# Kernel tuning notes

Hardware: AMD Instinct MI355X
Metric: run time of the kernel (lower is better)

Reference implementation:

```python
import jax, jax.numpy as jnp
import numpy as np

SEQ = 4096
NUM_INP = 1024
NUM_OUT = 128
NUM_HEADS = 8
NUM_HIDDEN = 64  # hardcoded in __init__
LN_EPS = 1e-5


def setup_inputs() -> dict:
    key = jax.random.key(0)
    ks = jax.random.split(key, 7)
    d_kq = NUM_HEADS * NUM_HIDDEN
    d_v = NUM_HEADS * NUM_OUT
    lim = 1.0 / np.sqrt(NUM_INP)
    return {
        "x": jax.random.normal(ks[0], (SEQ, NUM_INP), dtype=jnp.float32),
        "Wk": jax.random.uniform(ks[1], (d_kq, NUM_INP), jnp.float32, -lim, lim),
        "bk": jax.random.uniform(ks[2], (d_kq,), jnp.float32, -lim, lim),
        "Wq": jax.random.uniform(ks[3], (d_kq, NUM_INP), jnp.float32, -lim, lim),
        "bq": jax.random.uniform(ks[4], (d_kq,), jnp.float32, -lim, lim),
        "Wv": jax.random.uniform(ks[5], (d_v, NUM_INP), jnp.float32, -lim, lim),
        "bv": jax.random.uniform(ks[6], (d_v,), jnp.float32, -lim, lim),
        "ln_w": jnp.ones((NUM_OUT,), jnp.float32),
        "ln_b": jnp.zeros((NUM_OUT,), jnp.float32),
    }


def reference(x, Wk, bk, Wq, bq, Wv, bv, ln_w, ln_b):
    S = x.shape[0]
    # projections (eqx.nn.Linear: y = W @ x + b)
    k = (x @ Wk.T + bk).reshape(S, NUM_HEADS, NUM_HIDDEN)
    k = k / jnp.sqrt(jnp.asarray(NUM_HIDDEN, k.dtype))
    q = (x @ Wq.T + bq).reshape(S, NUM_HEADS, NUM_HIDDEN)
    v = (x @ Wv.T + bv).reshape(S, NUM_HEADS, NUM_OUT)
    # logits[i, j, h] = sum_k keys[i,h,k] * queries[j,h,k]
    logits = jnp.einsum('ihk,jhk->ijh', k, q)
    # softmax over axis=1 (the j / query axis, as in the original)
    attn = jax.nn.softmax(logits, axis=1)
    # contract over j AND heads -> [S, NUM_OUT]
    out = jnp.einsum('ijh,jhe->ie', attn, v)
    # LayerNorm over last dim with affine params
    mu = jnp.mean(out, axis=-1, keepdims=True)
    var = jnp.var(out, axis=-1, keepdims=True)
    normed = (out - mu) / jnp.sqrt(var + LN_EPS)
    return normed * ln_w + ln_b
```

## Files before the change

kernel.cpp:

```cpp
#include <hip/hip_runtime.h>
#include <hip/hip_bf16.h>

#define SEQ   4096
#define NINP  1024
#define NH    8
#define ND    64
#define NE    128
#define DKQ   512
#define DV    1024

typedef __attribute__((ext_vector_type(8))) short  short8;
typedef __attribute__((ext_vector_type(4))) float  floatx4;
typedef __attribute__((ext_vector_type(4))) unsigned short ushortx4;

__device__ __forceinline__ unsigned short f2bf(float f) {
    union { float f; unsigned int i; } v; v.f = f;
    unsigned int r = v.i + 0x7fffu + ((v.i >> 16) & 1u);
    return (unsigned short)(r >> 16);
}
__device__ __forceinline__ unsigned int pkperm(float hi, float lo) {
    return __builtin_amdgcn_perm(__float_as_uint(hi), __float_as_uint(lo), 0x07060302u);
}
__device__ __forceinline__ short8 pk8p(float4 a, float4 b) {
    int4 w;
    w.x = (int)pkperm(a.y, a.x);
    w.y = (int)pkperm(a.w, a.z);
    w.z = (int)pkperm(b.y, b.x);
    w.w = (int)pkperm(b.w, b.z);
    return *(short8*)&w;
}
__device__ __forceinline__ floatx4 mfma16(short8 a, short8 b, floatx4 c) {
    return __builtin_amdgcn_mfma_f32_16x16x32_bf16(a, b, c, 0, 0, 0);
}

__global__ __launch_bounds__(256)
void conv_kernel(const float* __restrict__ x,  const float* __restrict__ Wk,
                 const float* __restrict__ Wq, const float* __restrict__ Wv,
                 unsigned short* __restrict__ xbf,  unsigned short* __restrict__ Wkbf,
                 unsigned short* __restrict__ Wqbf, unsigned short* __restrict__ Wvbf)
{
    size_t idx = (size_t)blockIdx.x * 256 + threadIdx.x;
    const float* src; unsigned short* dst; size_t off;
    if      (idx < 524288)  { src = x;  dst = xbf;  off = idx; }
    else if (idx < 589824)  { src = Wk; dst = Wkbf; off = idx - 524288; }
    else if (idx < 655360)  { src = Wq; dst = Wqbf; off = idx - 589824; }
    else                    { src = Wv; dst = Wvbf; off = idx - 655360; }
    float4 a = *(const float4*)(src + off * 8);
    float4 b = *(const float4*)(src + off * 8 + 4);
    *(short8*)(dst + off * 8) = pk8p(a, b);
}

__global__ __launch_bounds__(256, 2)
void proj_kernel(const unsigned short* __restrict__ xbf,
                 const unsigned short* __restrict__ Wkbf, const float* __restrict__ bk,
                 const unsigned short* __restrict__ Wqbf, const float* __restrict__ bq,
                 const unsigned short* __restrict__ Wvbf, const float* __restrict__ bvv,
                 unsigned short* __restrict__ Kbuf, unsigned short* __restrict__ Qfrag,
                 unsigned short* __restrict__ Vfrag)
{
    __shared__ unsigned short As[128][72];
    __shared__ unsigned short Bs[128][72];

    const int ct = blockIdx.x;
    const int m0 = blockIdx.y * 128;

    const unsigned short* W; const float* bias;
    int colbase; float scale; int dest;
    if (ct < 4)      { W = Wkbf; bias = bk;  colbase = ct * 128;       scale = 0.18033688f; dest = 0; }
    else if (ct < 8) { W = Wqbf; bias = bq;  colbase = (ct - 4) * 128; scale = 1.0f;        dest = 1; }
    else             { W = Wvbf; bias = bvv; colbase = (ct - 8) * 128; scale = 1.0f;        dest = 2; }

    const int tid  = threadIdx.x;
    const int wv   = tid >> 6;
    const int lane = tid & 63;
    const int n    = lane & 15;
    const int qd   = lane >> 4;
    const int wr   = wv >> 1, wc = wv & 1;
    const int sr   = tid >> 1;
    const int skc  = (tid & 1) * 32;

    const unsigned short* xa0 = xbf + (size_t)(m0 + sr) * NINP + skc;
    const unsigned short* wb0 = W + (size_t)(colbase + sr) * NINP + skc;

    floatx4 acc[4][4] = {};
    short8 px[4], pw[4];

    #pragma unroll
    for (int c = 0; c < 4; ++c) {
        px[c] = *(const short8*)(xa0 + c*8);
        pw[c] = *(const short8*)(wb0 + c*8);
    }

    for (int k0 = 0; k0 < NINP; k0 += 64) {
        #pragma unroll
        for (int c = 0; c < 4; ++c) {
            *(short8*)&As[sr][skc + c*8] = px[c];
            *(short8*)&Bs[sr][skc + c*8] = pw[c];
        }
        const int kn = (k0 + 64 < NINP) ? k0 + 64 : k0;
        #pragma unroll
        for (int c = 0; c < 4; ++c) {
            px[c] = *(const short8*)(xa0 + kn + c*8);
            pw[c] = *(const short8*)(wb0 + kn + c*8);
        }
        __syncthreads();
        #pragma unroll
        for (int kk = 0; kk < 2; ++kk) {
            short8 af[4], bf4[4];
            #pragma unroll
            for (int mi = 0; mi < 4; ++mi)
                af[mi] = *(const short8*)&As[wr*64 + mi*16 + n][kk*32 + qd*8];
            #pragma unroll
            for (int ni = 0; ni < 4; ++ni)
                bf4[ni] = *(const short8*)&Bs[wc*64 + ni*16 + n][kk*32 + qd*8];
            #pragma unroll
            for (int mi = 0; mi < 4; ++mi)
                #pragma unroll
                for (int ni = 0; ni < 4; ++ni)
                    acc[mi][ni] = mfma16(af[mi], bf4[ni], acc[mi][ni]);
        }
        __syncthreads();
    }

    #pragma unroll
    for (int mi = 0; mi < 4; ++mi) {
        #pragma unroll
        for (int ni = 0; ni < 4; ++ni) {
            int o = colbase + wc*64 + ni*16 + n;
            float bfv = bias[o];
            int srow = m0 + wr*64 + mi*16 + qd*4;
            if (dest == 2) {
                int hh = o >> 7, e = o & 127;
                int e16 = e >> 4, ne = e & 15;
                int jt = srow >> 5, qd_a = (srow >> 3) & 3, t0 = srow & 7;
                ushortx4 pkv;
                #pragma unroll
                for (int r = 0; r < 4; ++r) pkv[r] = f2bf(acc[mi][ni][r] + bfv);
                *(ushortx4*)(Vfrag + (((size_t)hh*128 + jt)*8 + e16)*512
                             + (qd_a*16 + ne)*8 + t0) = pkv;
            } else if (dest == 1) {
                int hh = o >> 6, d = o & 63;
                int dd = d >> 5, qd_l = (d >> 3) & 3, t = d & 7;
                int jt = srow >> 5, a = (srow >> 4) & 1;
                size_t base = (((size_t)hh*128 + jt)*4 + (a + 2*dd))*512 + t;
                #pragma unroll
                for (int r = 0; r < 4; ++r) {
                    int nl = (srow + r) & 15;
                    Qfrag[base + (qd_l*16 + nl)*8] = f2bf(acc[mi][ni][r] + bfv);
                }
            } else {
                #pragma unroll
                for (int r = 0; r < 4; ++r)
                    Kbuf[(size_t)(srow + r) * DKQ + o] = f2bf((acc[mi][ni][r] + bfv) * scale);
            }
        }
    }
}

__global__ __launch_bounds__(256, 4)
void attn_kernel(const unsigned short* __restrict__ Kbuf,
                 const unsigned short* __restrict__ Qfrag,
                 const unsigned short* __restrict__ Vfrag,
                 float* __restrict__ Obuf,
                 float* dout)
{
    __shared__ unsigned char smem[34816];
    float* Red  = (float*)smem;
    float* DenS = (float*)(smem + 2 * 32 * 132 * 4);

    const int b    = blockIdx.x;
    const int h    = b & 7;
    const int i0   = (b >> 3) * 32;
    const int tid  = threadIdx.x;
    const int j_q  = tid >> 6;
    const int lane = tid & 63;
    const int n    = lane & 15;
    const int qd   = lane >> 4;

    short8 kf[2][2];
    #pragma unroll
    for (int g = 0; g < 2; ++g)
        #pragma unroll
        for (int d = 0; d < 2; ++d)
            kf[g][d] = *(const short8*)(Kbuf + (size_t)(i0 + g*16 + n) * DKQ
                                        + h * ND + d*32 + qd*8);

    floatx4 acc[8][2] = {};
    float den[2] = {0.f, 0.f};

    const int adA = (((qd & 1) << 5) + n) * 4;
    const int adB = adA + 64;
    const bool lo = (qd < 2);

    const unsigned short* Qbase = Qfrag + (size_t)h * 128 * 4 * 512 + lane * 8;
    const unsigned short* Vbase = Vfrag + (size_t)h * 128 * 8 * 512 + lane * 8;

    for (int k = 0; k < 32; ++k) {
        const int jt = j_q * 32 + k;

        const unsigned short* Qb = Qbase + (size_t)jt * 4 * 512;
        short8 qf00 = *(const short8*)(Qb);
        short8 qf10 = *(const short8*)(Qb + 512);
        short8 qf01 = *(const short8*)(Qb + 1024);
        short8 qf11 = *(const short8*)(Qb + 1536);
        const unsigned short* Vb = Vbase + (size_t)jt * 8 * 512;
        short8 vf[8];
        #pragma unroll
        for (int e16 = 0; e16 < 8; ++e16)
            vf[e16] = *(const short8*)(Vb + e16 * 512);

        floatx4 s[2][2] = {};
        #pragma unroll
        for (int g = 0; g < 2; ++g) {
            s[0][g] = mfma16(qf00, kf[g][0], s[0][g]); s[0][g] = mfma16(qf01, kf[g][1], s[0][g]);
            s[1][g] = mfma16(qf10, kf[g][0], s[1][g]); s[1][g] = mfma16(qf11, kf[g][1], s[1][g]);
        }

        int pkk[2][2][2];
        #pragma unroll
        for (int a = 0; a < 2; ++a)
            #pragma unroll
            for (int g = 0; g < 2; ++g) {
                float p0 = __builtin_amdgcn_exp2f(s[a][g][0]);
                float p1 = __builtin_amdgcn_exp2f(s[a][g][1]);
                float p2 = __builtin_amdgcn_exp2f(s[a][g][2]);
                float p3 = __builtin_amdgcn_exp2f(s[a][g][3]);
                den[g] += (p0 + p1) + (p2 + p3);
                pkk[a][g][0] = (int)pkperm(p1, p0);
                pkk[a][g][1] = (int)pkperm(p3, p2);
            }

        short8 bfrag[2];
        #pragma unroll
        for (int g = 0; g < 2; ++g) {
            int w0a = __builtin_amdgcn_ds_bpermute(adA, pkk[0][g][0]);
            int w1a = __builtin_amdgcn_ds_bpermute(adA, pkk[0][g][1]);
            int w2a = __builtin_amdgcn_ds_bpermute(adB, pkk[0][g][0]);
            int w3a = __builtin_amdgcn_ds_bpermute(adB, pkk[0][g][1]);
            int w0b = __builtin_amdgcn_ds_bpermute(adA, pkk[1][g][0]);
            int w1b = __builtin_amdgcn_ds_bpermute(adA, pkk[1][g][1]);
            int w2b = __builtin_amdgcn_ds_bpermute(adB, pkk[1][g][0]);
            int w3b = __builtin_amdgcn_ds_bpermute(adB, pkk[1][g][1]);
            int4 wv4;
            wv4.x = lo ? w0a : w0b;
            wv4.y = lo ? w1a : w1b;
            wv4.z = lo ? w2a : w2b;
            wv4.w = lo ? w3a : w3b;
            bfrag[g] = *(short8*)&wv4;
        }

        #pragma unroll
        for (int e16 = 0; e16 < 8; ++e16) {
            acc[e16][0] = mfma16(vf[e16], bfrag[0], acc[e16][0]);
            acc[e16][1] = mfma16(vf[e16], bfrag[1], acc[e16][1]);
        }
    }

    #pragma unroll
    for (int g = 0; g < 2; ++g) {
        den[g] += __shfl_xor(den[g], 16);
        den[g] += __shfl_xor(den[g], 32);
    }
    if (lane < 16) {
        DenS[j_q*32 + 0  + lane] = den[0];
        DenS[j_q*32 + 16 + lane] = den[1];
    }

    if (j_q >= 2) {
        #pragma unroll
        for (int e16 = 0; e16 < 8; ++e16)
            #pragma unroll
            for (int g = 0; g < 2; ++g)
                *(floatx4*)&Red[(j_q - 2)*32*132 + (g*16 + n)*132 + e16*16 + qd*4] = acc[e16][g];
    }
    __syncthreads();
    if (j_q == 1) {
        #pragma unroll
        for (int e16 = 0; e16 < 8; ++e16)
            #pragma unroll
            for (int g = 0; g < 2; ++g) {
                float* p = &Red[1*32*132 + (g*16 + n)*132 + e16*16 + qd*4];
                floatx4 o = *(const floatx4*)p;
                acc[e16][g][0] += o[0]; acc[e16][g][1] += o[1];
                acc[e16][g][2] += o[2]; acc[e16][g][3] += o[3];
                *(floatx4*)p = acc[e16][g];
            }
    } else if (j_q == 0) {
        #pragma unroll
        for (int e16 = 0; e16 < 8; ++e16)
            #pragma unroll
            for (int g = 0; g < 2; ++g) {
                floatx4 o = *(const floatx4*)&Red[0*32*132 + (g*16 + n)*132 + e16*16 + qd*4];
                acc[e16][g][0] += o[0]; acc[e16][g][1] += o[1];
                acc[e16][g][2] += o[2]; acc[e16][g][3] += o[3];
            }
    }
    __syncthreads();
    if (j_q == 0) {
        #pragma unroll
        for (int e16 = 0; e16 < 8; ++e16)
            #pragma unroll
            for (int g = 0; g < 2; ++g) {
                floatx4 o = *(const floatx4*)&Red[1*32*132 + (g*16 + n)*132 + e16*16 + qd*4];
                acc[e16][g][0] += o[0]; acc[e16][g][1] += o[1];
                acc[e16][g][2] += o[2]; acc[e16][g][3] += o[3];
                float* dst = Obuf + ((size_t)h * SEQ + i0 + g*16 + n) * NE + e16*16 + qd*4;
                *(floatx4*)dst = acc[e16][g];
            }
        if (lane < 32)
            dout[(size_t)(i0 + lane) * NE + h] =
                DenS[lane] + DenS[32 + lane] + DenS[64 + lane] + DenS[96 + lane];
    }
}

__global__ __launch_bounds__(256)
void ln_kernel(const float* __restrict__ Obuf,
               const float* __restrict__ lnA,
               const float* __restrict__ lnB,
               float* out)
{
    const bool aIsW = (lnA[0] == 1.0f);
    const float* lw = aIsW ? lnA : lnB;
    const float* lb = aIsW ? lnB : lnA;

    const int i    = blockIdx.x * 4 + (threadIdx.x >> 6);
    const int lane = threadIdx.x & 63;
    const int e0   = lane * 2;

    float inv[8];
    #pragma unroll
    for (int h = 0; h < 8; ++h) inv[h] = 1.0f / out[(size_t)i * NE + h];

    float x0 = 0.f, x1 = 0.f;
    #pragma unroll
    for (int h = 0; h < 8; ++h) {
        const float* p = Obuf + ((size_t)h * SEQ + i) * NE + e0;
        x0 += p[0] * inv[h]; x1 += p[1] * inv[h];
    }
    float s = x0 + x1, s2 = x0*x0 + x1*x1;
    #pragma unroll
    for (int off = 1; off < 64; off <<= 1) {
        s  += __shfl_xor(s,  off);
        s2 += __shfl_xor(s2, off);
    }
    float mu   = s * (1.f / 128.f);
    float var  = s2 * (1.f / 128.f) - mu * mu;
    float rstd = rsqrtf(var + 1e-5f);
    float2 y;
    y.x = (x0 - mu) * rstd * lw[e0]     + lb[e0];
    y.y = (x1 - mu) * rstd * lw[e0 + 1] + lb[e0 + 1];
    *(float2*)(out + (size_t)i * NE + e0) = y;
}

extern "C" void kernel_launch(void* const* d_in, const int* in_sizes, int n_in,
                              void* d_out, int out_size, void* d_ws, size_t ws_size,
                              hipStream_t stream)
{
    long long smax = 0;
    for (int i = 0; i < n_in; ++i) if ((long long)in_sizes[i] > smax) smax = in_sizes[i];
    const float *x = nullptr, *Wk = nullptr, *Wq = nullptr, *Wv = nullptr;
    const float *bk = nullptr, *bq = nullptr, *bv = nullptr, *lnA = nullptr, *lnB = nullptr;
    for (int i = 0; i < n_in; ++i) {
        long long s = in_sizes[i];
        const float* p = (const float*)d_in[i];
        if      (s == smax)          { x = p; }
        else if (s * 4 == smax)      { Wv = p; }
        else if (s * 8 == smax)      { if (!Wk) Wk = p; else Wq = p; }
        else if (s * 4096 == smax)   { bv = p; }
        else if (s * 8192 == smax)   { if (!bk) bk = p; else bq = p; }
        else if (s * 32768 == smax)  { if (!lnA) lnA = p; else lnB = p; }
    }

    unsigned short* Kbuf  = (unsigned short*)d_ws;
    unsigned short* Qfrag = Kbuf + (size_t)SEQ * DKQ;
    unsigned short* Vfrag = Qfrag + (size_t)SEQ * DKQ;
    unsigned short* xbf   = Vfrag + (size_t)NH * NE * SEQ;
    unsigned short* Wkbf  = xbf + (size_t)SEQ * NINP;
    unsigned short* Wqbf  = Wkbf + (size_t)DKQ * NINP;
    unsigned short* Wvbf  = Wqbf + (size_t)DKQ * NINP;
    float*          Obuf  = (float*)xbf;
    float*          out   = (float*)d_out;

    conv_kernel<<<dim3(3072), 256, 0, stream>>>(x, Wk, Wq, Wv, xbf, Wkbf, Wqbf, Wvbf);
    proj_kernel<<<dim3(16, 32), 256, 0, stream>>>(xbf, Wkbf, bk, Wqbf, bq, Wvbf, bv,
                                                  Kbuf, Qfrag, Vfrag);
    attn_kernel<<<dim3(1024), 256, 0, stream>>>(Kbuf, Qfrag, Vfrag, Obuf, out);
    ln_kernel<<<dim3(1024), 256, 0, stream>>>(Obuf, lnA, lnB, out);
}
```

Before: 203.3 us.

## Double attention row tile per block to reuse Q/V fragments across 64 rows

Each attention block now covers 64 key rows instead of 32, halving the grid to 512 blocks. The Q and V fragments loaded per j-tile are therefore reused across four row groups, halving global/L2 traffic for Q and V. The cross-wave reduction is split into two column halves so the shared-memory footprint stays about the same. The price is more accumulator registers, a lower occupancy target (launch bounds 2), and fewer blocks to spread across the CUs.

New measurement: 171.3 us. 1.19x faster.

```diff
diff --git a/kernel.cpp b/kernel.cpp
--- a/kernel.cpp
+++ b/kernel.cpp
@@ -157,36 +157,37 @@
     }
 }
 
-__global__ __launch_bounds__(256, 4)
+__global__ __launch_bounds__(256, 2)
 void attn_kernel(const unsigned short* __restrict__ Kbuf,
                  const unsigned short* __restrict__ Qfrag,
                  const unsigned short* __restrict__ Vfrag,
                  float* __restrict__ Obuf,
                  float* dout)
 {
-    __shared__ unsigned char smem[34816];
-    float* Red  = (float*)smem;
-    float* DenS = (float*)(smem + 2 * 32 * 132 * 4);
+    __shared__ unsigned char smem[35840];
+    float* Red0 = (float*)smem;
+    float* Red1 = Red0 + 64 * 68;
+    float* DenS = Red1 + 64 * 68;
 
     const int b    = blockIdx.x;
     const int h    = b & 7;
-    const int i0   = (b >> 3) * 32;
+    const int i0   = (b >> 3) * 64;
     const int tid  = threadIdx.x;
     const int j_q  = tid >> 6;
     const int lane = tid & 63;
     const int n    = lane & 15;
     const int qd   = lane >> 4;
 
-    short8 kf[2][2];
-    #pragma unroll
-    for (int g = 0; g < 2; ++g)
+    short8 kf[4][2];
+    #pragma unroll
+    for (int g = 0; g < 4; ++g)
         #pragma unroll
         for (int d = 0; d < 2; ++d)
             kf[g][d] = *(const short8*)(Kbuf + (size_t)(i0 + g*16 + n) * DKQ
                                         + h * ND + d*32 + qd*8);
 
-    floatx4 acc[8][2] = {};
-    float den[2] = {0.f, 0.f};
+    floatx4 acc[8][4] = {};
+    float den[4] = {0.f, 0.f, 0.f, 0.f};
 
     const int adA = (((qd & 1) << 5) + n) * 4;
     const int adB = adA + 64;
@@ -198,118 +199,131 @@
     for (int k = 0; k < 32; ++k) {
         const int jt = j_q * 32 + k;
 
-        const unsigned short* Qb = Qbase + (size_t)jt * 4 * 512;
+        const unsigned short* Qb = Qbase + (size_t)jt * 2048;
         short8 qf00 = *(const short8*)(Qb);
         short8 qf10 = *(const short8*)(Qb + 512);
         short8 qf01 = *(const short8*)(Qb + 1024);
         short8 qf11 = *(const short8*)(Qb + 1536);
-        const unsigned short* Vb = Vbase + (size_t)jt * 8 * 512;
+        const unsigned short* Vb = Vbase + (size_t)jt * 4096;
         short8 vf[8];
         #pragma unroll
         for (int e16 = 0; e16 < 8; ++e16)
             vf[e16] = *(const short8*)(Vb + e16 * 512);
 
-        floatx4 s[2][2] = {};
-        #pragma unroll
-        for (int g = 0; g < 2; ++g) {
-            s[0][g] = mfma16(qf00, kf[g][0], s[0][g]); s[0][g] = mfma16(qf01, kf[g][1], s[0][g]);
-            s[1][g] = mfma16(qf10, kf[g][0], s[1][g]); s[1][g] = mfma16(qf11, kf[g][1], s[1][g]);
-        }
-
-        int pkk[2][2][2];
-        #pragma unroll
-        for (int a = 0; a < 2; ++a)
-            #pragma unroll
-            for (int g = 0; g < 2; ++g) {
-                float p0 = __builtin_amdgcn_exp2f(s[a][g][0]);
-                float p1 = __builtin_amdgcn_exp2f(s[a][g][1]);
-                float p2 = __builtin_amdgcn_exp2f(s[a][g][2]);
-                float p3 = __builtin_amdgcn_exp2f(s[a][g][3]);
-                den[g] += (p0 + p1) + (p2 + p3);
-                pkk[a][g][0] = (int)pkperm(p1, p0);
-                pkk[a][g][1] = (int)pkperm(p3, p2);
+        #pragma unroll
+        for (int gc = 0; gc < 2; ++gc) {
+            floatx4 s[2][2] = {};
+            #pragma unroll
+            for (int gi = 0; gi < 2; ++gi) {
+                const int g = gc*2 + gi;
+                s[0][gi] = mfma16(qf00, kf[g][0], s[0][gi]); s[0][gi] = mfma16(qf01, kf[g][1], s[0][gi]);
+                s[1][gi] = mfma16(qf10, kf[g][0], s[1][gi]); s[1][gi] = mfma16(qf11, kf[g][1], s[1][gi]);
             }
 
-        short8 bfrag[2];
-        #pragma unroll
-        for (int g = 0; g < 2; ++g) {
-            int w0a = __builtin_amdgcn_ds_bpermute(adA, pkk[0][g][0]);
-            int w1a = __builtin_amdgcn_ds_bpermute(adA, pkk[0][g][1]);
-            int w2a = __builtin_amdgcn_ds_bpermute(adB, pkk[0][g][0]);
-            int w3a = __builtin_amdgcn_ds_bpermute(adB, pkk[0][g][1]);
-            int w0b = __builtin_amdgcn_ds_bpermute(adA, pkk[1][g][0]);
-            int w1b = __builtin_amdgcn_ds_bpermute(adA, pkk[1][g][1]);
-            int w2b = __builtin_amdgcn_ds_bpermute(adB, pkk[1][g][0]);
-            int w3b = __builtin_amdgcn_ds_bpermute(adB, pkk[1][g][1]);
-            int4 wv4;
-            wv4.x = lo ? w0a : w0b;
-            wv4.y = lo ? w1a : w1b;
-            wv4.z = lo ? w2a : w2b;
-            wv4.w = lo ? w3a : w3b;
-            bfrag[g] = *(short8*)&wv4;
-        }
-
-        #pragma unroll
-        for (int e16 = 0; e16 < 8; ++e16) {
-            acc[e16][0] = mfma16(vf[e16], bfrag[0], acc[e16][0]);
-            acc[e16][1] = mfma16(vf[e16], bfrag[1], acc[e16][1]);
-        }
-    }
-
-    #pragma unroll
-    for (int g = 0; g < 2; ++g) {
+            int pkk[2][2][2];
+            #pragma unroll
+            for (int a = 0; a < 2; ++a)
+                #pragma unroll
+                for (int gi = 0; gi < 2; ++gi) {
+                    float p0 = __builtin_amdgcn_exp2f(s[a][gi][0]);
+                    float p1 = __builtin_amdgcn_exp2f(s[a][gi][1]);
+                    float p2 = __builtin_amdgcn_exp2f(s[a][gi][2]);
+                    float p3 = __builtin_amdgcn_exp2f(s[a][gi][3]);
+                    den[gc*2 + gi] += (p0 + p1) + (p2 + p3);
+                    pkk[a][gi][0] = (int)pkperm(p1, p0);
+                    pkk[a][gi][1] = (int)pkperm(p3, p2);
+                }
+
+            short8 bfrag[2];
+            #pragma unroll
+            for (int gi = 0; gi < 2; ++gi) {
+                int w0a = __builtin_amdgcn_ds_bpermute(adA, pkk[0][gi][0]);
+                int w1a = __builtin_amdgcn_ds_bpermute(adA, pkk[0][gi][1]);
+                int w2a = __builtin_amdgcn_ds_bpermute(adB, pkk[0][gi][0]);
+                int w3a = __builtin_amdgcn_ds_bpermute(adB, pkk[0][gi][1]);
+                int w0b = __builtin_amdgcn_ds_bpermute(adA, pkk[1][gi][0]);
+                int w1b = __builtin_amdgcn_ds_bpermute(adA, pkk[1][gi][1]);
+                int w2b = __builtin_amdgcn_ds_bpermute(adB, pkk[1][gi][0]);
+                int w3b = __builtin_amdgcn_ds_bpermute(adB, pkk[1][gi][1]);
+                int4 wv4;
+                wv4.x = lo ? w0a : w0b;
+                wv4.y = lo ? w1a : w1b;
+                wv4.z = lo ? w2a : w2b;
+                wv4.w = lo ? w3a : w3b;
+                bfrag[gi] = *(short8*)&wv4;
+            }
+
+            #pragma unroll
+            for (int e16 = 0; e16 < 8; ++e16) {
+                acc[e16][gc*2]     = mfma16(vf[e16], bfrag[0], acc[e16][gc*2]);
+                acc[e16][gc*2 + 1] = mfma16(vf[e16], bfrag[1], acc[e16][gc*2 + 1]);
+            }
+        }
+    }
+
+    #pragma unroll
+    for (int g = 0; g < 4; ++g) {
         den[g] += __shfl_xor(den[g], 16);
         den[g] += __shfl_xor(den[g], 32);
     }
     if (lane < 16) {
-        DenS[j_q*32 + 0  + lane] = den[0];
-        DenS[j_q*32 + 16 + lane] = den[1];
-    }
-
-    if (j_q >= 2) {
-        #pragma unroll
-        for (int e16 = 0; e16 < 8; ++e16)
-            #pragma unroll
-            for (int g = 0; g < 2; ++g)
-                *(floatx4*)&Red[(j_q - 2)*32*132 + (g*16 + n)*132 + e16*16 + qd*4] = acc[e16][g];
-    }
-    __syncthreads();
-    if (j_q == 1) {
-        #pragma unroll
-        for (int e16 = 0; e16 < 8; ++e16)
-            #pragma unroll
-            for (int g = 0; g < 2; ++g) {
-                float* p = &Red[1*32*132 + (g*16 + n)*132 + e16*16 + qd*4];
-                floatx4 o = *(const floatx4*)p;
-                acc[e16][g][0] += o[0]; acc[e16][g][1] += o[1];
-                acc[e16][g][2] += o[2]; acc[e16][g][3] += o[3];
-                *(floatx4*)p = acc[e16][g];
-            }
-    } else if (j_q == 0) {
-        #pragma unroll
-        for (int e16 = 0; e16 < 8; ++e16)
-            #pragma unroll
-            for (int g = 0; g < 2; ++g) {
-                floatx4 o = *(const floatx4*)&Red[0*32*132 + (g*16 + n)*132 + e16*16 + qd*4];
-                acc[e16][g][0] += o[0]; acc[e16][g][1] += o[1];
-                acc[e16][g][2] += o[2]; acc[e16][g][3] += o[3];
-            }
-    }
-    __syncthreads();
+        #pragma unroll
+        for (int g = 0; g < 4; ++g)
+            DenS[j_q*64 + g*16 + lane] = den[g];
+    }
+
+    #pragma unroll
+    for (int eh = 0; eh < 2; ++eh) {
+        if (eh) __syncthreads();
+        if (j_q >= 2) {
+            float* Rb = (j_q == 2) ? Red0 : Red1;
+            #pragma unroll
+            for (int e = 0; e < 4; ++e)
+                #pragma unroll
+                for (int g = 0; g < 4; ++g)
+                    *(floatx4*)&Rb[(g*16 + n)*68 + e*16 + qd*4] = acc[eh*4 + e][g];
+        }
+        __syncthreads();
+        if (j_q == 1) {
+            #pragma unroll
+            for (int e = 0; e < 4; ++e)
+                #pragma unroll
+                for (int g = 0; g < 4; ++g) {
+                    float* p = &Red1[(g*16 + n)*68 + e*16 + qd*4];
+                    floatx4 o = *(const floatx4*)p;
+                    floatx4 r = acc[eh*4 + e][g];
+                    r[0] += o[0]; r[1] += o[1]; r[2] += o[2]; r[3] += o[3];
+                    *(floatx4*)p = r;
+                }
+        } else if (j_q == 0) {
+            #pragma unroll
+            for (int e = 0; e < 4; ++e)
+                #pragma unroll
+                for (int g = 0; g < 4; ++g) {
+                    floatx4 o = *(const floatx4*)&Red0[(g*16 + n)*68 + e*16 + qd*4];
+                    acc[eh*4 + e][g][0] += o[0]; acc[eh*4 + e][g][1] += o[1];
+                    acc[eh*4 + e][g][2] += o[2]; acc[eh*4 + e][g][3] += o[3];
+                }
+        }
+        __syncthreads();
+        if (j_q == 0) {
+            #pragma unroll
+            for (int e = 0; e < 4; ++e)
+                #pragma unroll
+                for (int g = 0; g < 4; ++g) {
+                    floatx4 o = *(const floatx4*)&Red1[(g*16 + n)*68 + e*16 + qd*4];
+                    floatx4 r = acc[eh*4 + e][g];
+                    r[0] += o[0]; r[1] += o[1]; r[2] += o[2]; r[3] += o[3];
+                    float* dst = Obuf + ((size_t)h * SEQ + i0 + g*16 + n) * NE
+                                 + (eh*4 + e)*16 + qd*4;
+                    *(floatx4*)dst = r;
+                }
+        }
+    }
+
     if (j_q == 0) {
-        #pragma unroll
-        for (int e16 = 0; e16 < 8; ++e16)
-            #pragma unroll
-            for (int g = 0; g < 2; ++g) {
-                floatx4 o = *(const floatx4*)&Red[1*32*132 + (g*16 + n)*132 + e16*16 + qd*4];
-                acc[e16][g][0] += o[0]; acc[e16][g][1] += o[1];
-                acc[e16][g][2] += o[2]; acc[e16][g][3] += o[3];
-                float* dst = Obuf + ((size_t)h * SEQ + i0 + g*16 + n) * NE + e16*16 + qd*4;
-                *(floatx4*)dst = acc[e16][g];
-            }
-        if (lane < 32)
-            dout[(size_t)(i0 + lane) * NE + h] =
-                DenS[lane] + DenS[32 + lane] + DenS[64 + lane] + DenS[96 + lane];
+        dout[(size_t)(i0 + lane) * NE + h] =
+            DenS[lane] + DenS[64 + lane] + DenS[128 + lane] + DenS[192 + lane];
     }
 }
 
@@ -384,6 +398,6 @@
     conv_kernel<<<dim3(3072), 256, 0, stream>>>(x, Wk, Wq, Wv, xbf, Wkbf, Wqbf, Wvbf);
     proj_kernel<<<dim3(16, 32), 256, 0, stream>>>(xbf, Wkbf, bk, Wqbf, bq, Wvbf, bv,
                                                   Kbuf, Qfrag, Vfrag);
-    attn_kernel<<<dim3(1024), 256, 0, stream>>>(Kbuf, Qfrag, Vfrag, Obuf, out);
+    attn_kernel<<<dim3(512), 256, 0, stream>>>(Kbuf, Qfrag, Vfrag, Obuf, out);
     ln_kernel<<<dim3(1024), 256, 0, stream>>>(Obuf, lnA, lnB, out);
 }
```

## Give each attention wave its own query rows over all keys, drop LDS reduction

Applied to the files above, without the earlier changes.

Before, the four waves of a block split the j (key) range and combined their partial outputs through shared memory with two barriers. Now each wave owns a distinct 16-row slice of a 64-row block and walks all 128 key tiles, so the LDS reduction and syncs disappear and the grid is halved. Q and V fragment loads are double-buffered in registers to overlap the next tile's loads with the current tile's MFMAs. The costs are that each wave reads the full Q/V stream for its head, occupancy is lowered to 2 blocks per unit, and the K fragment is no longer shared between two row groups per wave.

Measured after the change: 256.6 us. 1.26x slower.

```diff
diff --git a/kernel.cpp b/kernel.cpp
--- a/kernel.cpp
+++ b/kernel.cpp
@@ -157,160 +157,103 @@
     }
 }
 
-__global__ __launch_bounds__(256, 4)
+__global__ __launch_bounds__(256, 2)
 void attn_kernel(const unsigned short* __restrict__ Kbuf,
                  const unsigned short* __restrict__ Qfrag,
                  const unsigned short* __restrict__ Vfrag,
                  float* __restrict__ Obuf,
                  float* dout)
 {
-    __shared__ unsigned char smem[34816];
-    float* Red  = (float*)smem;
-    float* DenS = (float*)(smem + 2 * 32 * 132 * 4);
-
     const int b    = blockIdx.x;
     const int h    = b & 7;
-    const int i0   = (b >> 3) * 32;
+    const int i0   = (b >> 3) * 64;
     const int tid  = threadIdx.x;
-    const int j_q  = tid >> 6;
+    const int g    = tid >> 6;
     const int lane = tid & 63;
     const int n    = lane & 15;
     const int qd   = lane >> 4;
 
-    short8 kf[2][2];
-    #pragma unroll
-    for (int g = 0; g < 2; ++g)
-        #pragma unroll
-        for (int d = 0; d < 2; ++d)
-            kf[g][d] = *(const short8*)(Kbuf + (size_t)(i0 + g*16 + n) * DKQ
-                                        + h * ND + d*32 + qd*8);
-
-    floatx4 acc[8][2] = {};
-    float den[2] = {0.f, 0.f};
+    short8 kf[2];
+    #pragma unroll
+    for (int d = 0; d < 2; ++d)
+        kf[d] = *(const short8*)(Kbuf + (size_t)(i0 + g*16 + n) * DKQ
+                                 + h * ND + d*32 + qd*8);
+
+    floatx4 acc[8] = {};
+    float den = 0.f;
 
     const int adA = (((qd & 1) << 5) + n) * 4;
     const int adB = adA + 64;
     const bool lo = (qd < 2);
 
-    const unsigned short* Qbase = Qfrag + (size_t)h * 128 * 4 * 512 + lane * 8;
-    const unsigned short* Vbase = Vfrag + (size_t)h * 128 * 8 * 512 + lane * 8;
-
-    for (int k = 0; k < 32; ++k) {
-        const int jt = j_q * 32 + k;
-
-        const unsigned short* Qb = Qbase + (size_t)jt * 4 * 512;
-        short8 qf00 = *(const short8*)(Qb);
-        short8 qf10 = *(const short8*)(Qb + 512);
-        short8 qf01 = *(const short8*)(Qb + 1024);
-        short8 qf11 = *(const short8*)(Qb + 1536);
-        const unsigned short* Vb = Vbase + (size_t)jt * 8 * 512;
-        short8 vf[8];
+    const unsigned short* Qbase = Qfrag + (size_t)h * (128*4*512) + lane * 8;
+    const unsigned short* Vbase = Vfrag + (size_t)h * (128*8*512) + lane * 8;
+
+    short8 qA[4], vA[8], qB[4], vB[8];
+
+    auto fetch = [&](short8 (&qf)[4], short8 (&vf)[8], int jt) {
+        const unsigned short* Qb = Qbase + (size_t)jt * 2048;
+        const unsigned short* Vb = Vbase + (size_t)jt * 4096;
+        #pragma unroll
+        for (int f = 0; f < 4; ++f) qf[f] = *(const short8*)(Qb + f * 512);
+        #pragma unroll
+        for (int e = 0; e < 8; ++e) vf[e] = *(const short8*)(Vb + e * 512);
+    };
+
+    auto compute = [&](const short8 (&qf)[4], const short8 (&vf)[8]) {
+        floatx4 s[2] = {};
+        s[0] = mfma16(qf[0], kf[0], s[0]); s[0] = mfma16(qf[2], kf[1], s[0]);
+        s[1] = mfma16(qf[1], kf[0], s[1]); s[1] = mfma16(qf[3], kf[1], s[1]);
+
+        int pkk[2][2];
+        #pragma unroll
+        for (int a = 0; a < 2; ++a) {
+            float p0 = __builtin_amdgcn_exp2f(s[a][0]);
+            float p1 = __builtin_amdgcn_exp2f(s[a][1]);
+            float p2 = __builtin_amdgcn_exp2f(s[a][2]);
+            float p3 = __builtin_amdgcn_exp2f(s[a][3]);
+            den += (p0 + p1) + (p2 + p3);
+            pkk[a][0] = (int)pkperm(p1, p0);
+            pkk[a][1] = (int)pkperm(p3, p2);
+        }
+
+        int w0a = __builtin_amdgcn_ds_bpermute(adA, pkk[0][0]);
+        int w1a = __builtin_amdgcn_ds_bpermute(adA, pkk[0][1]);
+        int w2a = __builtin_amdgcn_ds_bpermute(adB, pkk[0][0]);
+        int w3a = __builtin_amdgcn_ds_bpermute(adB, pkk[0][1]);
+        int w0b = __builtin_amdgcn_ds_bpermute(adA, pkk[1][0]);
+        int w1b = __builtin_amdgcn_ds_bpermute(adA, pkk[1][1]);
+        int w2b = __builtin_amdgcn_ds_bpermute(adB, pkk[1][0]);
+        int w3b = __builtin_amdgcn_ds_bpermute(adB, pkk[1][1]);
+        int4 wv4;
+        wv4.x = lo ? w0a : w0b;
+        wv4.y = lo ? w1a : w1b;
+        wv4.z = lo ? w2a : w2b;
+        wv4.w = lo ? w3a : w3b;
+        short8 bfrag = *(short8*)&wv4;
+
         #pragma unroll
         for (int e16 = 0; e16 < 8; ++e16)
-            vf[e16] = *(const short8*)(Vb + e16 * 512);
-
-        floatx4 s[2][2] = {};
-        #pragma unroll
-        for (int g = 0; g < 2; ++g) {
-            s[0][g] = mfma16(qf00, kf[g][0], s[0][g]); s[0][g] = mfma16(qf01, kf[g][1], s[0][g]);
-            s[1][g] = mfma16(qf10, kf[g][0], s[1][g]); s[1][g] = mfma16(qf11, kf[g][1], s[1][g]);
-        }
-
-        int pkk[2][2][2];
-        #pragma unroll
-        for (int a = 0; a < 2; ++a)
-            #pragma unroll
-            for (int g = 0; g < 2; ++g) {
-                float p0 = __builtin_amdgcn_exp2f(s[a][g][0]);
-                float p1 = __builtin_amdgcn_exp2f(s[a][g][1]);
-                float p2 = __builtin_amdgcn_exp2f(s[a][g][2]);
-                float p3 = __builtin_amdgcn_exp2f(s[a][g][3]);
-                den[g] += (p0 + p1) + (p2 + p3);
-                pkk[a][g][0] = (int)pkperm(p1, p0);
-                pkk[a][g][1] = (int)pkperm(p3, p2);
-            }
-
-        short8 bfrag[2];
-        #pragma unroll
-        for (int g = 0; g < 2; ++g) {
-            int w0a = __builtin_amdgcn_ds_bpermute(adA, pkk[0][g][0]);
-            int w1a = __builtin_amdgcn_ds_bpermute(adA, pkk[0][g][1]);
-            int w2a = __builtin_amdgcn_ds_bpermute(adB, pkk[0][g][0]);
-            int w3a = __builtin_amdgcn_ds_bpermute(adB, pkk[0][g][1]);
-            int w0b = __builtin_amdgcn_ds_bpermute(adA, pkk[1][g][0]);
-            int w1b = __builtin_amdgcn_ds_bpermute(adA, pkk[1][g][1]);
-            int w2b = __builtin_amdgcn_ds_bpermute(adB, pkk[1][g][0]);
-            int w3b = __builtin_amdgcn_ds_bpermute(adB, pkk[1][g][1]);
-            int4 wv4;
-            wv4.x = lo ? w0a : w0b;
-            wv4.y = lo ? w1a : w1b;
-            wv4.z = lo ? w2a : w2b;
-            wv4.w = lo ? w3a : w3b;
-            bfrag[g] = *(short8*)&wv4;
-        }
-
-        #pragma unroll
-        for (int e16 = 0; e16 < 8; ++e16) {
-            acc[e16][0] = mfma16(vf[e16], bfrag[0], acc[e16][0]);
-            acc[e16][1] = mfma16(vf[e16], bfrag[1], acc[e16][1]);
-        }
-    }
-
-    #pragma unroll
-    for (int g = 0; g < 2; ++g) {
-        den[g] += __shfl_xor(den[g], 16);
-        den[g] += __shfl_xor(den[g], 32);
-    }
-    if (lane < 16) {
-        DenS[j_q*32 + 0  + lane] = den[0];
-        DenS[j_q*32 + 16 + lane] = den[1];
-    }
-
-    if (j_q >= 2) {
-        #pragma unroll
-        for (int e16 = 0; e16 < 8; ++e16)
-            #pragma unroll
-            for (int g = 0; g < 2; ++g)
-                *(floatx4*)&Red[(j_q - 2)*32*132 + (g*16 + n)*132 + e16*16 + qd*4] = acc[e16][g];
-    }
-    __syncthreads();
-    if (j_q == 1) {
-        #pragma unroll
-        for (int e16 = 0; e16 < 8; ++e16)
-            #pragma unroll
-            for (int g = 0; g < 2; ++g) {
-                float* p = &Red[1*32*132 + (g*16 + n)*132 + e16*16 + qd*4];
-                floatx4 o = *(const floatx4*)p;
-                acc[e16][g][0] += o[0]; acc[e16][g][1] += o[1];
-                acc[e16][g][2] += o[2]; acc[e16][g][3] += o[3];
-                *(floatx4*)p = acc[e16][g];
-            }
-    } else if (j_q == 0) {
-        #pragma unroll
-        for (int e16 = 0; e16 < 8; ++e16)
-            #pragma unroll
-            for (int g = 0; g < 2; ++g) {
-                floatx4 o = *(const floatx4*)&Red[0*32*132 + (g*16 + n)*132 + e16*16 + qd*4];
-                acc[e16][g][0] += o[0]; acc[e16][g][1] += o[1];
-                acc[e16][g][2] += o[2]; acc[e16][g][3] += o[3];
-            }
-    }
-    __syncthreads();
-    if (j_q == 0) {
-        #pragma unroll
-        for (int e16 = 0; e16 < 8; ++e16)
-            #pragma unroll
-            for (int g = 0; g < 2; ++g) {
-                floatx4 o = *(const floatx4*)&Red[1*32*132 + (g*16 + n)*132 + e16*16 + qd*4];
-                acc[e16][g][0] += o[0]; acc[e16][g][1] += o[1];
-                acc[e16][g][2] += o[2]; acc[e16][g][3] += o[3];
-                float* dst = Obuf + ((size_t)h * SEQ + i0 + g*16 + n) * NE + e16*16 + qd*4;
-                *(floatx4*)dst = acc[e16][g];
-            }
-        if (lane < 32)
-            dout[(size_t)(i0 + lane) * NE + h] =
-                DenS[lane] + DenS[32 + lane] + DenS[64 + lane] + DenS[96 + lane];
-    }
+            acc[e16] = mfma16(vf[e16], bfrag, acc[e16]);
+    };
+
+    fetch(qA, vA, 0);
+    for (int jt = 0; jt < 128; jt += 2) {
+        fetch(qB, vB, jt + 1);
+        compute(qA, vA);
+        fetch(qA, vA, (jt + 2 < 128) ? jt + 2 : jt);
+        compute(qB, vB);
+    }
+
+    den += __shfl_xor(den, 16);
+    den += __shfl_xor(den, 32);
+    if (lane < 16)
+        dout[(size_t)(i0 + g*16 + lane) * NE + h] = den;
+
+    #pragma unroll
+    for (int e16 = 0; e16 < 8; ++e16)
+        *(floatx4*)(Obuf + ((size_t)h * SEQ + i0 + g*16 + n) * NE + e16*16 + qd*4)
+            = acc[e16];
 }
 
 __global__ __launch_bounds__(256)
@@ -384,6 +327,6 @@
     conv_kernel<<<dim3(3072), 256, 0, stream>>>(x, Wk, Wq, Wv, xbf, Wkbf, Wqbf, Wvbf);
     proj_kernel<<<dim3(16, 32), 256, 0, stream>>>(xbf, Wkbf, bk, Wqbf, bq, Wvbf, bv,
                                                   Kbuf, Qfrag, Vfrag);
-    attn_kernel<<<dim3(1024), 256, 0, stream>>>(Kbuf, Qfrag, Vfrag, Obuf, out);
+    attn_kernel<<<dim3(512), 256, 0, stream>>>(Kbuf, Qfrag, Vfrag, Obuf, out);
     ln_kernel<<<dim3(1024), 256, 0, stream>>>(Obuf, lnA, lnB, out);
 }
```

## Double attention block to 64 rows and split LDS reduction into halves

Applied to the files above, without the earlier changes.

The attention kernel now launches 512-thread blocks that each cover two 32-row query groups (8 waves: 2 row groups x 4 key-range waves). Waves in the same block that read the same Q/V fragments can share them through cache, and there are half as many blocks. The cross-wave reduction now runs in two halves over the output columns with a 68-float stride, so two row groups fit in about the same LDS as one did before. The cost is an extra barrier round per block, and a larger block may reduce scheduling flexibility and occupancy.

Result: no change. 201.2 us (-1.0%).

```diff
diff --git a/kernel.cpp b/kernel.cpp
--- a/kernel.cpp
+++ b/kernel.cpp
@@ -157,22 +157,24 @@
     }
 }
 
-__global__ __launch_bounds__(256, 4)
+__global__ __launch_bounds__(512, 4)
 void attn_kernel(const unsigned short* __restrict__ Kbuf,
                  const unsigned short* __restrict__ Qfrag,
                  const unsigned short* __restrict__ Vfrag,
                  float* __restrict__ Obuf,
                  float* dout)
 {
-    __shared__ unsigned char smem[34816];
+    __shared__ unsigned char smem[35840];
     float* Red  = (float*)smem;
-    float* DenS = (float*)(smem + 2 * 32 * 132 * 4);
+    float* DenS = (float*)(smem + 4 * 32 * 68 * 4);
 
     const int b    = blockIdx.x;
     const int h    = b & 7;
-    const int i0   = (b >> 3) * 32;
     const int tid  = threadIdx.x;
-    const int j_q  = tid >> 6;
+    const int w    = tid >> 6;
+    const int iq   = w >> 2;
+    const int jq   = w & 3;
+    const int i0   = (b >> 3) * 64 + iq * 32;
     const int lane = tid & 63;
     const int n    = lane & 15;
     const int qd   = lane >> 4;
@@ -196,14 +198,14 @@
     const unsigned short* Vbase = Vfrag + (size_t)h * 128 * 8 * 512 + lane * 8;
 
     for (int k = 0; k < 32; ++k) {
-        const int jt = j_q * 32 + k;
-
-        const unsigned short* Qb = Qbase + (size_t)jt * 4 * 512;
+        const int jt = jq * 32 + k;
+
+        const unsigned short* Qb = Qbase + (size_t)jt * 2048;
         short8 qf00 = *(const short8*)(Qb);
         short8 qf10 = *(const short8*)(Qb + 512);
         short8 qf01 = *(const short8*)(Qb + 1024);
         short8 qf11 = *(const short8*)(Qb + 1536);
-        const unsigned short* Vb = Vbase + (size_t)jt * 8 * 512;
+        const unsigned short* Vb = Vbase + (size_t)jt * 4096;
         short8 vf[8];
         #pragma unroll
         for (int e16 = 0; e16 < 8; ++e16)
@@ -262,54 +264,65 @@
         den[g] += __shfl_xor(den[g], 32);
     }
     if (lane < 16) {
-        DenS[j_q*32 + 0  + lane] = den[0];
-        DenS[j_q*32 + 16 + lane] = den[1];
-    }
-
-    if (j_q >= 2) {
-        #pragma unroll
-        for (int e16 = 0; e16 < 8; ++e16)
-            #pragma unroll
-            for (int g = 0; g < 2; ++g)
-                *(floatx4*)&Red[(j_q - 2)*32*132 + (g*16 + n)*132 + e16*16 + qd*4] = acc[e16][g];
-    }
-    __syncthreads();
-    if (j_q == 1) {
-        #pragma unroll
-        for (int e16 = 0; e16 < 8; ++e16)
-            #pragma unroll
-            for (int g = 0; g < 2; ++g) {
-                float* p = &Red[1*32*132 + (g*16 + n)*132 + e16*16 + qd*4];
-                floatx4 o = *(const floatx4*)p;
-                acc[e16][g][0] += o[0]; acc[e16][g][1] += o[1];
-                acc[e16][g][2] += o[2]; acc[e16][g][3] += o[3];
-                *(floatx4*)p = acc[e16][g];
-            }
-    } else if (j_q == 0) {
-        #pragma unroll
-        for (int e16 = 0; e16 < 8; ++e16)
-            #pragma unroll
-            for (int g = 0; g < 2; ++g) {
-                floatx4 o = *(const floatx4*)&Red[0*32*132 + (g*16 + n)*132 + e16*16 + qd*4];
-                acc[e16][g][0] += o[0]; acc[e16][g][1] += o[1];
-                acc[e16][g][2] += o[2]; acc[e16][g][3] += o[3];
-            }
-    }
-    __syncthreads();
-    if (j_q == 0) {
-        #pragma unroll
-        for (int e16 = 0; e16 < 8; ++e16)
-            #pragma unroll
-            for (int g = 0; g < 2; ++g) {
-                floatx4 o = *(const floatx4*)&Red[1*32*132 + (g*16 + n)*132 + e16*16 + qd*4];
-                acc[e16][g][0] += o[0]; acc[e16][g][1] += o[1];
-                acc[e16][g][2] += o[2]; acc[e16][g][3] += o[3];
-                float* dst = Obuf + ((size_t)h * SEQ + i0 + g*16 + n) * NE + e16*16 + qd*4;
-                *(floatx4*)dst = acc[e16][g];
-            }
-        if (lane < 32)
-            dout[(size_t)(i0 + lane) * NE + h] =
-                DenS[lane] + DenS[32 + lane] + DenS[64 + lane] + DenS[96 + lane];
+        DenS[w*32 + 0  + lane] = den[0];
+        DenS[w*32 + 16 + lane] = den[1];
+    }
+
+    float* R0 = Red + iq * (2 * 32 * 68);
+    float* R1 = R0 + 32 * 68;
+    #pragma unroll
+    for (int eh = 0; eh < 2; ++eh) {
+        if (eh) __syncthreads();
+        if (jq >= 2) {
+            float* Rb = (jq == 2) ? R0 : R1;
+            #pragma unroll
+            for (int e = 0; e < 4; ++e)
+                #pragma unroll
+                for (int g = 0; g < 2; ++g)
+                    *(floatx4*)&Rb[(g*16 + n)*68 + e*16 + qd*4] = acc[eh*4 + e][g];
+        }
+        __syncthreads();
+        if (jq == 1) {
+            #pragma unroll
+            for (int e = 0; e < 4; ++e)
+                #pragma unroll
+                for (int g = 0; g < 2; ++g) {
+                    float* p = &R1[(g*16 + n)*68 + e*16 + qd*4];
+                    floatx4 o = *(const floatx4*)p;
+                    floatx4 r = acc[eh*4 + e][g];
+                    r[0] += o[0]; r[1] += o[1]; r[2] += o[2]; r[3] += o[3];
+                    *(floatx4*)p = r;
+                }
+        } else if (jq == 0) {
+            #pragma unroll
+            for (int e = 0; e < 4; ++e)
+                #pragma unroll
+                for (int g = 0; g < 2; ++g) {
+                    floatx4 o = *(const floatx4*)&R0[(g*16 + n)*68 + e*16 + qd*4];
+                    acc[eh*4 + e][g][0] += o[0]; acc[eh*4 + e][g][1] += o[1];
+                    acc[eh*4 + e][g][2] += o[2]; acc[eh*4 + e][g][3] += o[3];
+                }
+        }
+        __syncthreads();
+        if (jq == 0) {
+            #pragma unroll
+            for (int e = 0; e < 4; ++e)
+                #pragma unroll
+                for (int g = 0; g < 2; ++g) {
+                    floatx4 o = *(const floatx4*)&R1[(g*16 + n)*68 + e*16 + qd*4];
+                    floatx4 r = acc[eh*4 + e][g];
+                    r[0] += o[0]; r[1] += o[1]; r[2] += o[2]; r[3] += o[3];
+                    float* dst = Obuf + ((size_t)h * SEQ + i0 + g*16 + n) * NE
+                                 + (eh*4 + e)*16 + qd*4;
+                    *(floatx4*)dst = r;
+                }
+        }
+    }
+
+    if (jq == 0 && lane < 32) {
+        dout[(size_t)(i0 + lane) * NE + h] =
+            DenS[(iq*4 + 0)*32 + lane] + DenS[(iq*4 + 1)*32 + lane] +
+            DenS[(iq*4 + 2)*32 + lane] + DenS[(iq*4 + 3)*32 + lane];
     }
 }
 
@@ -384,6 +397,6 @@
     conv_kernel<<<dim3(3072), 256, 0, stream>>>(x, Wk, Wq, Wv, xbf, Wkbf, Wqbf, Wvbf);
     proj_kernel<<<dim3(16, 32), 256, 0, stream>>>(xbf, Wkbf, bk, Wqbf, bq, Wvbf, bv,
                                                   Kbuf, Qfrag, Vfrag);
-    attn_kernel<<<dim3(1024), 256, 0, stream>>>(Kbuf, Qfrag, Vfrag, Obuf, out);
+    attn_kernel<<<dim3(512), 512, 0, stream>>>(Kbuf, Qfrag, Vfrag, Obuf, out);
     ln_kernel<<<dim3(1024), 256, 0, stream>>>(Obuf, lnA, lnB, out);
 }
```
